# Kernel tuning notes

Measured on AMD Instinct MI355X. Metric: run time of the kernel, lower is better.

Reference implementation:

```python
import jax, jax.numpy as jnp
import numpy as np

B, S, D, NH = 2, 1024, 512, 16  # batch, seq_len, d_model, num_heads (chunk size!)
C = D // NH  # number of chunks produced by torch split(num_heads, dim=-1)


def _split_heads(x):
    # torch: torch.stack(x.split(NH, dim=-1)) -> (C, B, S, NH), chunk i = cols [i*NH:(i+1)*NH]
    b, s, d = x.shape
    return jnp.moveaxis(x.reshape(b, s, C, NH), 2, 0)


def setup_inputs() -> dict:
    key = jax.random.key(0)
    ks = jax.random.split(key, 7)
    mk = lambda k, shp, scale=1.0: (jax.random.normal(k, shp, dtype=jnp.float32) * scale)
    return {
        "Q": mk(ks[0], (B, S, D)),
        "K": mk(ks[1], (B, S, D)),
        "V": mk(ks[2], (B, S, D)),
        "Wq": mk(ks[3], (D, D), D ** -0.5),
        "Wk": mk(ks[4], (D, D), D ** -0.5),
        "Wv": mk(ks[5], (D, D), D ** -0.5),
        "Wo": mk(ks[6], (D, D), D ** -0.5),
    }


def reference(Q, K, V, Wq, Wk, Wv, Wo):
    # bias-free linear projections (torch Linear: x @ W.T)
    q = Q @ Wq.T
    k = K @ Wk.T
    v = V @ Wv.T
    qh, kh, vh = _split_heads(q), _split_heads(k), _split_heads(v)  # (C, B, S, NH)
    # NOTE: scale is sqrt(Q.size(-1)) = sqrt(num_heads), faithful to source
    scale = jnp.sqrt(jnp.asarray(float(NH), dtype=qh.dtype))
    scores = jnp.einsum("cbmh,cbnh->cbmn", qh, kh) / scale  # (C, B, S, S)
    weights = jax.nn.softmax(scores, axis=-1)
    att = jnp.einsum("cbmn,cbnh->cbmh", weights, vh)  # (C, B, S, NH)
    # faithful to torch permute(0,2,1,3) then reshape(batch, -1, d_model)
    out = att.transpose(0, 2, 1, 3).reshape(B, -1, D)
    out = out @ Wo.T
    return (out, weights)
```

## Files before the change

kernel.cpp:

```cpp
#include <hip/hip_runtime.h>
#include <cstdint>
#include <cstddef>


typedef __attribute__((ext_vector_type(8)))  short    short8;
typedef __attribute__((ext_vector_type(4)))  float    f32x4;
typedef __attribute__((ext_vector_type(4)))  unsigned u32x4;

union FragU { u32x4 u; short8 s; };

__device__ __forceinline__ unsigned pk_bf16(float a, float b) {
    unsigned ua = __float_as_uint(a), ub = __float_as_uint(b);
    ua = (ua + 0x7fffu + ((ua >> 16) & 1u)) >> 16;
    ub = (ub + 0x7fffu + ((ub >> 16) & 1u)) >> 16;
    return ua | (ub << 16);
}

__device__ __forceinline__ void gemm_nt_mfma_body(const float* __restrict__ X,
                                                  const float* __restrict__ W,
                                                  float* __restrict__ P)
{
    __shared__ unsigned Xs[64 * 33 * 4];
    __shared__ unsigned Ws[64 * 33 * 4];
    const int t  = threadIdx.x;
    const int m0 = blockIdx.y << 6;
    const int n0 = blockIdx.x << 6;
    const int wave = t >> 6, lane = t & 63;
    const int ml = lane & 15;
    const int g  = lane >> 4;

    f32x4 acc[4] = {{0,0,0,0}, {0,0,0,0}, {0,0,0,0}, {0,0,0,0}};

#pragma unroll 1
    for (int kh = 0; kh < 2; ++kh) {
        if (kh) __syncthreads();
#pragma unroll
        for (int rep = 0; rep < 8; ++rep) {
            int f  = rep * 256 + t;
            int kf = f & 31, r = f >> 5;
            const float* xr = X + (size_t)(m0 + r) * 512 + kh * 256 + kf * 8;
            float4 a = *(const float4*)xr;
            float4 b = *(const float4*)(xr + 4);
            unsigned* dx = &Xs[(r * 33 + kf) * 4];
            dx[0] = pk_bf16(a.x, a.y); dx[1] = pk_bf16(a.z, a.w);
            dx[2] = pk_bf16(b.x, b.y); dx[3] = pk_bf16(b.z, b.w);
            const float* wr = W + (size_t)(n0 + r) * 512 + kh * 256 + kf * 8;
            float4 c = *(const float4*)wr;
            float4 d = *(const float4*)(wr + 4);
            unsigned* dw = &Ws[(r * 33 + kf) * 4];
            dw[0] = pk_bf16(c.x, c.y); dw[1] = pk_bf16(c.z, c.w);
            dw[2] = pk_bf16(d.x, d.y); dw[3] = pk_bf16(d.z, d.w);
        }
        __syncthreads();
#pragma unroll
        for (int ks = 0; ks < 8; ++ks) {
            const int kf = ks * 4 + g;
            FragU a;
            a.u = *(const u32x4*)&Xs[((wave * 16 + ml) * 33 + kf) * 4];
#pragma unroll
            for (int nf = 0; nf < 4; ++nf) {
                FragU bw;
                bw.u = *(const u32x4*)&Ws[((nf * 16 + ml) * 33 + kf) * 4];
                acc[nf] = __builtin_amdgcn_mfma_f32_16x16x32_bf16(
                    a.s, bw.s, acc[nf], 0, 0, 0);
            }
        }
    }
#pragma unroll
    for (int nf = 0; nf < 4; ++nf) {
#pragma unroll
        for (int r = 0; r < 4; ++r) {
            const int m = m0 + wave * 16 + g * 4 + r;
            P[(size_t)m * 512 + n0 + nf * 16 + ml] = acc[nf][r];
        }
    }
}

__global__ __launch_bounds__(256, 2) void proj3_kernel(
    const float* __restrict__ Q, const float* __restrict__ K, const float* __restrict__ V,
    const float* __restrict__ Wq, const float* __restrict__ Wk, const float* __restrict__ Wv,
    float* __restrict__ q, float* __restrict__ k, float* __restrict__ v)
{
    const float* X; const float* W; float* P;
    if (blockIdx.z == 0)      { X = Q; W = Wq; P = q; }
    else if (blockIdx.z == 1) { X = K; W = Wk; P = k; }
    else                      { X = V; W = Wv; P = v; }
    gemm_nt_mfma_body(X, W, P);
}

__global__ __launch_bounds__(256, 2) void outproj_kernel(
    const float* __restrict__ att, const float* __restrict__ Wo, float* __restrict__ out)
{
    gemm_nt_mfma_body(att, Wo, out);
}

__global__ __launch_bounds__(512)
void attn_mfma_kernel(
    const float* __restrict__ q, const float* __restrict__ k, const float* __restrict__ v,
    float* __restrict__ wts, float* __restrict__ att)
{
    __shared__ unsigned ksF[64 * 128];
    __shared__ unsigned vsT[16][514];
    __shared__ unsigned pbuf[8][16][18];

    const int t     = threadIdx.x;
    const int bid   = blockIdx.x;
    const int strip = bid & 7;
    const int cb    = bid >> 3;
    const int b     = cb & 1;
    const int c     = cb >> 1;
    const int m0b   = strip << 7;

    const float* kb = k + (size_t)b * 524288 + c * 16;
    const float* vb = v + (size_t)b * 524288 + c * 16;

#pragma unroll
    for (int rep = 0; rep < 4; ++rep) {
        int f = rep * 512 + t;
        int n = f >> 1, gg = f & 1;
        const float* kr = kb + (size_t)n * 512 + gg * 8;
        float4 a  = *(const float4*)kr;
        float4 bq = *(const float4*)(kr + 4);
        unsigned* dst = &ksF[(n >> 4) * 128 + ((n & 15) + (gg << 4)) * 4];
        dst[0] = pk_bf16(a.x, a.y);
        dst[1] = pk_bf16(a.z, a.w);
        dst[2] = pk_bf16(bq.x, bq.y);
        dst[3] = pk_bf16(bq.z, bq.w);
    }
#pragma unroll
    for (int rep = 0; rep < 4; ++rep) {
        int f = rep * 512 + t;
        int p = f >> 2, hq = f & 3;
        float4 v0 = *(const float4*)(vb + (size_t)(2 * p)     * 512 + hq * 4);
        float4 v1 = *(const float4*)(vb + (size_t)(2 * p + 1) * 512 + hq * 4);
        vsT[hq * 4 + 0][p] = pk_bf16(v0.x, v1.x);
        vsT[hq * 4 + 1][p] = pk_bf16(v0.y, v1.y);
        vsT[hq * 4 + 2][p] = pk_bf16(v0.z, v1.z);
        vsT[hq * 4 + 3][p] = pk_bf16(v0.w, v1.w);
    }
    __syncthreads();

    const int wave = t >> 6, lane = t & 63;
    const int ml = lane & 15;
    const int g  = lane >> 4;
    const int m0w = m0b + wave * 16;

    FragU qf;
    if (g < 2) {
        const float* qr = q + (size_t)b * 524288
                            + (size_t)(m0w + ml) * 512 + c * 16 + g * 8;
        float4 a  = *(const float4*)qr;
        float4 bq = *(const float4*)(qr + 4);
        qf.u[0] = pk_bf16(a.x * 0.25f, a.y * 0.25f);
        qf.u[1] = pk_bf16(a.z * 0.25f, a.w * 0.25f);
        qf.u[2] = pk_bf16(bq.x * 0.25f, bq.y * 0.25f);
        qf.u[3] = pk_bf16(bq.z * 0.25f, bq.w * 0.25f);
    } else {
        qf.u = (u32x4){0, 0, 0, 0};
    }

    const f32x4 zero4 = {0.f, 0.f, 0.f, 0.f};

    float rs = 0.f;
#pragma unroll 1
    for (int nt = 0; nt < 64; ++nt) {
        FragU ka;
        if (lane < 32) ka.u = *(const u32x4*)&ksF[nt * 128 + lane * 4];
        else           ka.u = (u32x4){0, 0, 0, 0};
        f32x4 st = __builtin_amdgcn_mfma_f32_16x16x32_bf16(ka.s, qf.s, zero4, 0, 0, 0);
        rs += (__expf(st[0]) + __expf(st[1])) + (__expf(st[2]) + __expf(st[3]));
    }
    rs += __shfl_xor(rs, 16);
    rs += __shfl_xor(rs, 32);
    const float inv = 1.0f / rs;

    f32x4 acc = zero4;
    float* wrow = wts + (size_t)cb * 1048576 + (size_t)(m0w + ml) * 1024;
#pragma unroll 1
    for (int ntp = 0; ntp < 32; ++ntp) {
#pragma unroll
        for (int sub = 0; sub < 2; ++sub) {
            const int nt = ntp * 2 + sub;
            FragU ka;
            if (lane < 32) ka.u = *(const u32x4*)&ksF[nt * 128 + lane * 4];
            else           ka.u = (u32x4){0, 0, 0, 0};
            f32x4 st = __builtin_amdgcn_mfma_f32_16x16x32_bf16(ka.s, qf.s, zero4, 0, 0, 0);
            float w0 = __expf(st[0]) * inv;
            float w1 = __expf(st[1]) * inv;
            float w2 = __expf(st[2]) * inv;
            float w3 = __expf(st[3]) * inv;
            *(float4*)(wrow + nt * 16 + g * 4) = make_float4(w0, w1, w2, w3);
            unsigned* pb = &pbuf[wave][ml][sub * 8 + g * 2];
            pb[0] = pk_bf16(w0, w1);
            pb[1] = pk_bf16(w2, w3);
        }
        FragU pa, vf;
        pa.u = *(const u32x4*)&pbuf[wave][ml][g * 4];
        vf.u = *(const u32x4*)&vsT[ml][ntp * 16 + g * 4];
        acc = __builtin_amdgcn_mfma_f32_16x16x32_bf16(pa.s, vf.s, acc, 0, 0, 0);
    }

    const int b2 = c >> 4;
#pragma unroll
    for (int r = 0; r < 4; ++r) {
        const int m  = m0w + g * 4 + r;
        const int m2 = (c & 15) * 64 + (m >> 4);
        const int d2 = (m & 15) * 32 + b * 16 + ml;
        att[((size_t)b2 * 1024 + m2) * 512 + d2] = acc[r];
    }
}

extern "C" void kernel_launch(void* const* d_in, const int* in_sizes, int n_in,
                              void* d_out, int out_size, void* d_ws, size_t ws_size,
                              hipStream_t stream)
{
    (void)in_sizes; (void)n_in; (void)out_size; (void)ws_size;
    const float* Q  = (const float*)d_in[0];
    const float* K  = (const float*)d_in[1];
    const float* V  = (const float*)d_in[2];
    const float* Wq = (const float*)d_in[3];
    const float* Wk = (const float*)d_in[4];
    const float* Wv = (const float*)d_in[5];
    const float* Wo = (const float*)d_in[6];

    float* out = (float*)d_out;
    float* wts = out + 1048576;

    float* ws  = (float*)d_ws;
    float* q   = ws;
    float* k   = ws + (1u << 20);
    float* v   = ws + 2 * (1u << 20);
    float* att = ws + 3 * (1u << 20);

    proj3_kernel<<<dim3(8, 32, 3), 256, 0, stream>>>(Q, K, V, Wq, Wk, Wv, q, k, v);
    attn_mfma_kernel<<<512, 512, 0, stream>>>(q, k, v, wts, att);
    outproj_kernel<<<dim3(8, 32, 1), 256, 0, stream>>>(att, Wo, out);
}
```

Before: 105.3 us.

## Enlarge GEMM M-tile to 128 with 4-stage K loop and nontemporal weight stores

The projection GEMMs now use 128x64 tiles, with each wave computing two 16-row fragments so every loaded W fragment is reused twice. The K dimension is staged in four 128-wide chunks, keeping LDS usage small. Grid sizes are halved to match. Separately, the large attention-weights output is written with nontemporal stores so it does not pollute the cache. The larger tiles mean fewer blocks (384 and 128), which may underfill the GPU.

```diff
diff --git a/kernel.cpp b/kernel.cpp
--- a/kernel.cpp
+++ b/kernel.cpp
@@ -20,60 +20,70 @@
                                                   const float* __restrict__ W,
                                                   float* __restrict__ P)
 {
-    __shared__ unsigned Xs[64 * 33 * 4];
-    __shared__ unsigned Ws[64 * 33 * 4];
+    __shared__ unsigned Xs[128 * 17 * 4];
+    __shared__ unsigned Ws[64 * 17 * 4];
     const int t  = threadIdx.x;
-    const int m0 = blockIdx.y << 6;
+    const int m0 = blockIdx.y << 7;
     const int n0 = blockIdx.x << 6;
     const int wave = t >> 6, lane = t & 63;
     const int ml = lane & 15;
     const int g  = lane >> 4;
 
-    f32x4 acc[4] = {{0,0,0,0}, {0,0,0,0}, {0,0,0,0}, {0,0,0,0}};
+    f32x4 acc[2][4] = {{{0,0,0,0},{0,0,0,0},{0,0,0,0},{0,0,0,0}},
+                       {{0,0,0,0},{0,0,0,0},{0,0,0,0},{0,0,0,0}}};
 
 #pragma unroll 1
-    for (int kh = 0; kh < 2; ++kh) {
-        if (kh) __syncthreads();
+    for (int st = 0; st < 4; ++st) {
+        if (st) __syncthreads();
 #pragma unroll
         for (int rep = 0; rep < 8; ++rep) {
             int f  = rep * 256 + t;
-            int kf = f & 31, r = f >> 5;
-            const float* xr = X + (size_t)(m0 + r) * 512 + kh * 256 + kf * 8;
+            int kf = f & 15, r = f >> 4;
+            const float* xr = X + (size_t)(m0 + r) * 512 + st * 128 + kf * 8;
             float4 a = *(const float4*)xr;
             float4 b = *(const float4*)(xr + 4);
-            unsigned* dx = &Xs[(r * 33 + kf) * 4];
+            unsigned* dx = &Xs[(r * 17 + kf) * 4];
             dx[0] = pk_bf16(a.x, a.y); dx[1] = pk_bf16(a.z, a.w);
             dx[2] = pk_bf16(b.x, b.y); dx[3] = pk_bf16(b.z, b.w);
-            const float* wr = W + (size_t)(n0 + r) * 512 + kh * 256 + kf * 8;
+        }
+#pragma unroll
+        for (int rep = 0; rep < 4; ++rep) {
+            int f  = rep * 256 + t;
+            int kf = f & 15, r = f >> 4;
+            const float* wr = W + (size_t)(n0 + r) * 512 + st * 128 + kf * 8;
             float4 c = *(const float4*)wr;
             float4 d = *(const float4*)(wr + 4);
-            unsigned* dw = &Ws[(r * 33 + kf) * 4];
+            unsigned* dw = &Ws[(r * 17 + kf) * 4];
             dw[0] = pk_bf16(c.x, c.y); dw[1] = pk_bf16(c.z, c.w);
             dw[2] = pk_bf16(d.x, d.y); dw[3] = pk_bf16(d.z, d.w);
         }
         __syncthreads();
 #pragma unroll
-        for (int ks = 0; ks < 8; ++ks) {
+        for (int ks = 0; ks < 4; ++ks) {
             const int kf = ks * 4 + g;
-            FragU a;
-            a.u = *(const u32x4*)&Xs[((wave * 16 + ml) * 33 + kf) * 4];
+            FragU a0, a1;
+            a0.u = *(const u32x4*)&Xs[((wave * 32 + ml) * 17 + kf) * 4];
+            a1.u = *(const u32x4*)&Xs[((wave * 32 + 16 + ml) * 17 + kf) * 4];
 #pragma unroll
             for (int nf = 0; nf < 4; ++nf) {
                 FragU bw;
-                bw.u = *(const u32x4*)&Ws[((nf * 16 + ml) * 33 + kf) * 4];
-                acc[nf] = __builtin_amdgcn_mfma_f32_16x16x32_bf16(
-                    a.s, bw.s, acc[nf], 0, 0, 0);
+                bw.u = *(const u32x4*)&Ws[((nf * 16 + ml) * 17 + kf) * 4];
+                acc[0][nf] = __builtin_amdgcn_mfma_f32_16x16x32_bf16(
+                    a0.s, bw.s, acc[0][nf], 0, 0, 0);
+                acc[1][nf] = __builtin_amdgcn_mfma_f32_16x16x32_bf16(
+                    a1.s, bw.s, acc[1][nf], 0, 0, 0);
             }
         }
     }
 #pragma unroll
-    for (int nf = 0; nf < 4; ++nf) {
-#pragma unroll
-        for (int r = 0; r < 4; ++r) {
-            const int m = m0 + wave * 16 + g * 4 + r;
-            P[(size_t)m * 512 + n0 + nf * 16 + ml] = acc[nf][r];
-        }
-    }
+    for (int af = 0; af < 2; ++af)
+#pragma unroll
+        for (int nf = 0; nf < 4; ++nf)
+#pragma unroll
+            for (int r = 0; r < 4; ++r) {
+                const int m = m0 + wave * 32 + af * 16 + g * 4 + r;
+                P[(size_t)m * 512 + n0 + nf * 16 + ml] = acc[af][nf][r];
+            }
 }
 
 __global__ __launch_bounds__(256, 2) void proj3_kernel(
@@ -189,7 +199,9 @@
             float w1 = __expf(st[1]) * inv;
             float w2 = __expf(st[2]) * inv;
             float w3 = __expf(st[3]) * inv;
-            *(float4*)(wrow + nt * 16 + g * 4) = make_float4(w0, w1, w2, w3);
+            f32x4 w4 = {w0, w1, w2, w3};
+            __builtin_nontemporal_store(
+                w4, reinterpret_cast<f32x4*>(wrow + nt * 16 + g * 4));
             unsigned* pb = &pbuf[wave][ml][sub * 8 + g * 2];
             pb[0] = pk_bf16(w0, w1);
             pb[1] = pk_bf16(w2, w3);
@@ -232,7 +244,7 @@
     float* v   = ws + 2 * (1u << 20);
     float* att = ws + 3 * (1u << 20);
 
-    proj3_kernel<<<dim3(8, 32, 3), 256, 0, stream>>>(Q, K, V, Wq, Wk, Wv, q, k, v);
+    proj3_kernel<<<dim3(8, 16, 3), 256, 0, stream>>>(Q, K, V, Wq, Wk, Wv, q, k, v);
     attn_mfma_kernel<<<512, 512, 0, stream>>>(q, k, v, wts, att);
-    outproj_kernel<<<dim3(8, 32, 1), 256, 0, stream>>>(att, Wo, out);
-}
+    outproj_kernel<<<dim3(8, 16, 1), 256, 0, stream>>>(att, Wo, out);
+}
```

Measured after the change: 142.0 us. +34.9%, slower.
